# Optimization experiments

Hardware: AMD Instinct MI355X
Metric: run time of the kernel (lower is better)

Reference implementation:

```python
import jax, jax.numpy as jnp
import numpy as np

N_NODES = 100000
N_EDGES = 1600000
D_IN = 128
D_OUT = 128


def setup_inputs() -> dict:
    key = jax.random.key(0)
    k1, k2, k3, k4 = jax.random.split(key, 4)
    feat = jax.random.normal(k1, (N_NODES, D_IN), dtype=jnp.float32)
    W1 = jax.random.normal(k2, (D_OUT, D_IN), dtype=jnp.float32) * (1.0 / np.sqrt(D_IN))
    src = jax.random.randint(k3, (N_EDGES,), 0, N_NODES, dtype=jnp.int32)
    # ensure every dst node has at least one in-edge (no empty segments, like a
    # DGL graph without isolated destination nodes)
    dst_rand = jax.random.randint(k4, (N_EDGES - N_NODES,), 0, N_NODES, dtype=jnp.int32)
    dst = jnp.concatenate([jnp.arange(N_NODES, dtype=jnp.int32), dst_rand])
    return {"feat": feat, "W1": W1, "src": src, "dst": dst}


def reference(feat, W1, src, dst):
    # nn.Linear(bias=False): h = feat @ W1.T   -> [N, D_OUT]
    norm_h = jnp.einsum("nd,od->no", feat, W1)
    # copy_u message + max reduce: segment-max of projected src feats onto dst
    msgs = norm_h[src]                                   # [E, D_OUT] gather
    h_N = jax.ops.segment_max(msgs, dst, num_segments=feat.shape[0])  # [N, D_OUT]
    # concat(feat_dst, h_N) along feature dim
    return jnp.concatenate([feat, h_N], axis=1)          # [N, D_IN + D_OUT]
```

## Files before the change

kernel.cpp:

```cpp
#include <hip/hip_runtime.h>
#include <hip/hip_bf16.h>
#include <cfloat>

typedef short bf16x8 __attribute__((ext_vector_type(8)));
typedef float f32x4 __attribute__((ext_vector_type(4)));

constexpr int NB2     = 1600;
constexpr int PCHUNK  = 6144;
constexpr int NCH_MAX = 264;
constexpr int OFFROW  = 1604;
constexpr int BCAPK   = 2048;

__device__ __forceinline__ unsigned short f32_to_bf16_rne(float f) {
    unsigned int u = __float_as_uint(f);
    u += 0x7fffu + ((u >> 16) & 1u);
    return (unsigned short)(u >> 16);
}
__device__ __forceinline__ float b2f(unsigned int w, int k) {
    return (float)((int)(w << (24 - 8 * k)) >> 24);
}

__global__ __launch_bounds__(256) void ka_part_gemm_kernel(
    const float* __restrict__ feat, const float* __restrict__ W1,
    signed char* __restrict__ norm8, float* __restrict__ rowscale,
    float* __restrict__ out,
    const int* __restrict__ src, const int* __restrict__ dst,
    int* __restrict__ part, unsigned short* __restrict__ offRow,
    int N, int E, int partBlocks) {
    __shared__ __align__(16) char smem[35200];
    const int t = threadIdx.x;

    if ((int)blockIdx.x < partBlocks) {
        int* stage   = (int*)smem;
        int* pkCnt   = stage + PCHUNK;
        int* pkOff   = pkCnt + 800;
        int* pkLoc   = pkOff + 800;
        int* partial = pkLoc + 800;

        const int c0 = blockIdx.x * PCHUNK;
        const int n  = (E - c0 < PCHUNK) ? (E - c0) : PCHUNK;

        for (int i = t; i < 800; i += 256) pkCnt[i] = 0;
        __syncthreads();

#pragma unroll
        for (int j = 0; j < PCHUNK / 1024; ++j) {
            int i = (j * 256 + t) * 4;
            if (i + 3 < n) {
                int4 d4 = *(const int4*)(dst + c0 + i);
                atomicAdd(&pkCnt[(d4.x >> 6) >> 1], 1 << (((d4.x >> 6) & 1) << 4));
                atomicAdd(&pkCnt[(d4.y >> 6) >> 1], 1 << (((d4.y >> 6) & 1) << 4));
                atomicAdd(&pkCnt[(d4.z >> 6) >> 1], 1 << (((d4.z >> 6) & 1) << 4));
                atomicAdd(&pkCnt[(d4.w >> 6) >> 1], 1 << (((d4.w >> 6) & 1) << 4));
            } else if (i < n) {
                for (int k = i; k < n; ++k) {
                    int b = dst[c0 + k] >> 6;
                    atomicAdd(&pkCnt[b >> 1], 1 << ((b & 1) << 4));
                }
            }
        }
        __syncthreads();

        {
            int w0 = 0, w1 = 0, w2 = 0, w3 = 0;
            if (t < 200) {
                w0 = pkCnt[4 * t];     w1 = pkCnt[4 * t + 1];
                w2 = pkCnt[4 * t + 2]; w3 = pkCnt[4 * t + 3];
            }
            int cA = w0 & 0xFFFF, cB = (w0 >> 16) & 0xFFFF;
            int cC = w1 & 0xFFFF, cD = (w1 >> 16) & 0xFFFF;
            int cE = w2 & 0xFFFF, cF = (w2 >> 16) & 0xFFFF;
            int cG = w3 & 0xFFFF, cH = (w3 >> 16) & 0xFFFF;
            partial[t] = cA + cB + cC + cD + cE + cF + cG + cH;
            __syncthreads();
            for (int d = 1; d < 256; d <<= 1) {
                int x = (t >= d) ? partial[t - d] : 0;
                __syncthreads();
                if (t >= d) partial[t] += x;
                __syncthreads();
            }
            if (t < 200) {
                int run = t ? partial[t - 1] : 0;
                int o0 = run,      o1 = o0 + cA, o2 = o1 + cB, o3 = o2 + cC;
                int o4 = o3 + cD,  o5 = o4 + cE, o6 = o5 + cF, o7 = o6 + cG;
                pkOff[4 * t]     = o0 | (o1 << 16);
                pkOff[4 * t + 1] = o2 | (o3 << 16);
                pkOff[4 * t + 2] = o4 | (o5 << 16);
                pkOff[4 * t + 3] = o6 | (o7 << 16);
                pkLoc[4 * t]     = o0 | (o1 << 16);
                pkLoc[4 * t + 1] = o2 | (o3 << 16);
                pkLoc[4 * t + 2] = o4 | (o5 << 16);
                pkLoc[4 * t + 3] = o6 | (o7 << 16);
            }
        }
        __syncthreads();

#pragma unroll
        for (int j = 0; j < PCHUNK / 1024; ++j) {
            int i = (j * 256 + t) * 4;
            if (i + 3 < n) {
                int4 d4 = *(const int4*)(dst + c0 + i);
                int4 s4 = *(const int4*)(src + c0 + i);
                int b, sh, old;
                b = d4.x >> 6; sh = (b & 1) << 4;
                old = atomicAdd(&pkLoc[b >> 1], 1 << sh);
                stage[(old >> sh) & 0xFFFF] = s4.x | ((d4.x & 63) << 17);
                b = d4.y >> 6; sh = (b & 1) << 4;
                old = atomicAdd(&pkLoc[b >> 1], 1 << sh);
                stage[(old >> sh) & 0xFFFF] = s4.y | ((d4.y & 63) << 17);
                b = d4.z >> 6; sh = (b & 1) << 4;
                old = atomicAdd(&pkLoc[b >> 1], 1 << sh);
                stage[(old >> sh) & 0xFFFF] = s4.z | ((d4.z & 63) << 17);
                b = d4.w >> 6; sh = (b & 1) << 4;
                old = atomicAdd(&pkLoc[b >> 1], 1 << sh);
                stage[(old >> sh) & 0xFFFF] = s4.w | ((d4.w & 63) << 17);
            } else if (i < n) {
                for (int k = i; k < n; ++k) {
                    int d = dst[c0 + k];
                    int b = d >> 6, sh = (b & 1) << 4;
                    int old = atomicAdd(&pkLoc[b >> 1], 1 << sh);
                    stage[(old >> sh) & 0xFFFF] = src[c0 + k] | ((d & 63) << 17);
                }
            }
        }
        __syncthreads();

        for (int i = t * 4; i < n; i += 1024) {
            if (i + 3 < n) *(int4*)(part + c0 + i) = *(const int4*)(stage + i);
            else for (int k = i; k < n; ++k) part[c0 + k] = stage[k];
        }
        unsigned short* orow = offRow + (size_t)blockIdx.x * OFFROW;
        for (int b = t; b <= NB2; b += 256) {
            int v = (b < NB2) ? ((pkOff[b >> 1] >> ((b & 1) << 4)) & 0xFFFF) : n;
            orow[b] = (unsigned short)v;
        }
    } else {
        unsigned short* smW = (unsigned short*)smem;
#pragma unroll
        for (int i = 0; i < 8; ++i) {
            int f = i * 256 + t;
            int l = f & 63, kb = (f >> 6) & 3, ot = f >> 8;
            int wrow = ot * 16 + (l & 15);
            int k0 = kb * 32 + (l >> 4) * 8;
            const float* p = W1 + wrow * 128 + k0;
            float4 f0 = *(const float4*)p;
            float4 f1 = *(const float4*)(p + 4);
            union { unsigned short h[8]; uint4 v; } pk;
            pk.h[0] = f32_to_bf16_rne(f0.x); pk.h[1] = f32_to_bf16_rne(f0.y);
            pk.h[2] = f32_to_bf16_rne(f0.z); pk.h[3] = f32_to_bf16_rne(f0.w);
            pk.h[4] = f32_to_bf16_rne(f1.x); pk.h[5] = f32_to_bf16_rne(f1.y);
            pk.h[6] = f32_to_bf16_rne(f1.z); pk.h[7] = f32_to_bf16_rne(f1.w);
            *(uint4*)(smW + (size_t)f * 8) = pk.v;
        }

        const int bid = blockIdx.x - partBlocks;
        const int w = t >> 6;
        const int l = t & 63;
        const int brow0 = bid * 64;
        const int row = brow0 + w * 16 + (l & 15);
        const int kq = (l >> 4) * 8;
        const bool valid = row < N;

        bf16x8 a[4];
        const float* fr = feat + (size_t)row * 128;
        float* orow_ = out + (size_t)row * 256;
#pragma unroll
        for (int kb = 0; kb < 4; ++kb) {
            float4 f0 = make_float4(0.f, 0.f, 0.f, 0.f), f1 = f0;
            if (valid) {
                f0 = *(const float4*)(fr + kb * 32 + kq);
                f1 = *(const float4*)(fr + kb * 32 + kq + 4);
                *(float4*)(orow_ + kb * 32 + kq) = f0;
                *(float4*)(orow_ + kb * 32 + kq + 4) = f1;
            }
            bf16x8 av;
            av[0] = (short)f32_to_bf16_rne(f0.x); av[1] = (short)f32_to_bf16_rne(f0.y);
            av[2] = (short)f32_to_bf16_rne(f0.z); av[3] = (short)f32_to_bf16_rne(f0.w);
            av[4] = (short)f32_to_bf16_rne(f1.x); av[5] = (short)f32_to_bf16_rne(f1.y);
            av[6] = (short)f32_to_bf16_rne(f1.z); av[7] = (short)f32_to_bf16_rne(f1.w);
            a[kb] = av;
        }
        __syncthreads();

        const bf16x8* bfr = (const bf16x8*)smem;
        f32x4 zero = {0.f, 0.f, 0.f, 0.f};
        f32x4 acc[8];
#pragma unroll
        for (int ot = 0; ot < 8; ++ot) acc[ot] = zero;
#pragma unroll
        for (int ot = 0; ot < 8; ++ot) {
#pragma unroll
            for (int kb = 0; kb < 4; ++kb) {
                bf16x8 b = bfr[(ot * 4 + kb) * 64 + l];
                acc[ot] = __builtin_amdgcn_mfma_f32_16x16x32_bf16(a[kb], b, acc[ot], 0, 0, 0);
            }
        }

        const int r0 = w * 16 + (l >> 4) * 4;
        float inv[4], scl[4];
#pragma unroll
        for (int j = 0; j < 4; ++j) {
            float am = 0.f;
#pragma unroll
            for (int ot = 0; ot < 8; ++ot) am = fmaxf(am, __builtin_fabsf(acc[ot][j]));
#pragma unroll
            for (int d = 1; d < 16; d <<= 1) am = fmaxf(am, __shfl_xor(am, d, 64));
            am = fmaxf(am, 1e-30f);
            inv[j] = 127.0f / am;
            scl[j] = am * (1.0f / 127.0f);
        }
        if ((l & 15) == 0) {
#pragma unroll
            for (int j = 0; j < 4; ++j) {
                int grow = brow0 + r0 + j;
                if (grow < N) rowscale[grow] = scl[j];
            }
        }
        __syncthreads();

        char (*sm8)[144] = (char (*)[144])smem;
        const int c0 = l & 15;
#pragma unroll
        for (int ot = 0; ot < 8; ++ot)
#pragma unroll
            for (int j = 0; j < 4; ++j)
                sm8[r0 + j][ot * 16 + c0] = (char)(int)rintf(acc[ot][j] * inv[j]);
        __syncthreads();
#pragma unroll
        for (int i = 0; i < 2; ++i) {
            int idx = i * 256 + t;
            int r = idx >> 3, c = idx & 7;
            int grow = brow0 + r;
            if (grow < N) {
                uint4 v = *(const uint4*)&sm8[r][c * 16];
                *(uint4*)(norm8 + (size_t)grow * 128 + c * 16) = v;
            }
        }
    }
}

__global__ __launch_bounds__(256) void kb_maxpool_kernel(
    const signed char* __restrict__ norm8, const float* __restrict__ rowscale,
    const int* __restrict__ part, const unsigned short* __restrict__ offRow,
    float* __restrict__ out, int N, int nch) {
    __shared__ int eraw[BCAPK];
    __shared__ int esrc[BCAPK];
    __shared__ int runs_s[NCH_MAX];
    __shared__ int rlen[NCH_MAX + 1];
    __shared__ int eoff[65];
    __shared__ int eloc[64];

    const int B = blockIdx.x;
    const int t = threadIdx.x;

    for (int c = t; c < nch; c += 256) {
        const unsigned short* orow = offRow + (size_t)c * OFFROW;
        int s = orow[B];
        int e = orow[B + 1];
        runs_s[c] = s;
        rlen[c] = e - s;
    }
    if (t < 64) eloc[t] = 0;
    __syncthreads();
    if (t < 64) {
        int carry = 0;
        int rounds = (nch + 63) / 64;
        for (int r = 0; r < rounds; ++r) {
            int c = r * 64 + t;
            int orig = (c < nch) ? rlen[c] : 0;
            int v = orig;
#pragma unroll
            for (int d = 1; d < 64; d <<= 1) {
                int x = __shfl_up(v, d, 64);
                if (t >= d) v += x;
            }
            if (c < nch) rlen[c] = carry + v - orig;
            carry += __shfl(v, 63, 64);
        }
        if (t == 0) rlen[nch] = carry;
    }
    __syncthreads();
    int cnt = rlen[nch];
    if (cnt > BCAPK) cnt = BCAPK;

    {
        int g = t >> 4, ln = t & 15;
        for (int c = g; c < nch; c += 16) {
            int s = runs_s[c], d0 = rlen[c], l = rlen[c + 1] - rlen[c];
            const int* gp = part + (size_t)c * PCHUNK + s;
            for (int i = ln; i < l; i += 16) {
                int d = d0 + i;
                if (d < BCAPK) eraw[d] = gp[i];
            }
        }
    }
    __syncthreads();

    for (int i = t; i < cnt; i += 256) atomicAdd(&eloc[eraw[i] >> 17], 1);
    __syncthreads();
    if (t < 64) {
        int v = eloc[t];
        int sc = v;
#pragma unroll
        for (int d = 1; d < 64; d <<= 1) {
            int x = __shfl_up(sc, d, 64);
            if (t >= d) sc += x;
        }
        int excl = sc - v;
        eoff[t] = excl;
        eloc[t] = excl;
        if (t == 63) eoff[64] = sc;
    }
    __syncthreads();
    for (int i = t; i < cnt; i += 256) {
        int v = eraw[i];
        esrc[atomicAdd(&eloc[v >> 17], 1)] = v & 0x1FFFF;
    }
    __syncthreads();

    int qw = t >> 4;
    int ln = t & 15;
    const size_t colb = (size_t)ln * 8;
    for (int dl = qw; dl < 64; dl += 16) {
        int node = (B << 6) + dl;
        if (node >= N) break;
        int si = eoff[dl], se = eoff[dl + 1];
        if (se > BCAPK) se = BCAPK;
        float a0 = -FLT_MAX, a1 = -FLT_MAX, a2 = -FLT_MAX, a3 = -FLT_MAX;
        float a4 = -FLT_MAX, a5 = -FLT_MAX, a6 = -FLT_MAX, a7 = -FLT_MAX;
        float b0 = -FLT_MAX, b1 = -FLT_MAX, b2 = -FLT_MAX, b3 = -FLT_MAX;
        float b4 = -FLT_MAX, b5 = -FLT_MAX, b6 = -FLT_MAX, b7 = -FLT_MAX;
        float c0 = -FLT_MAX, c1 = -FLT_MAX, c2 = -FLT_MAX, c3 = -FLT_MAX;
        float c4 = -FLT_MAX, c5 = -FLT_MAX, c6 = -FLT_MAX, c7 = -FLT_MAX;
        float d0 = -FLT_MAX, d1 = -FLT_MAX, d2 = -FLT_MAX, d3 = -FLT_MAX;
        float d4 = -FLT_MAX, d5 = -FLT_MAX, d6 = -FLT_MAX, d7 = -FLT_MAX;
        int i = si;
        for (; i + 3 < se; i += 4) {
            int s1 = esrc[i], s2 = esrc[i + 1], s3 = esrc[i + 2], s4 = esrc[i + 3];
            uint2 wA = *(const uint2*)(norm8 + (size_t)s1 * 128 + colb);
            uint2 wB = *(const uint2*)(norm8 + (size_t)s2 * 128 + colb);
            uint2 wC = *(const uint2*)(norm8 + (size_t)s3 * 128 + colb);
            uint2 wD = *(const uint2*)(norm8 + (size_t)s4 * 128 + colb);
            float sA = rowscale[s1], sB = rowscale[s2];
            float sC = rowscale[s3], sD = rowscale[s4];
            a0 = fmaxf(a0, b2f(wA.x, 0) * sA); a1 = fmaxf(a1, b2f(wA.x, 1) * sA);
            a2 = fmaxf(a2, b2f(wA.x, 2) * sA); a3 = fmaxf(a3, b2f(wA.x, 3) * sA);
            a4 = fmaxf(a4, b2f(wA.y, 0) * sA); a5 = fmaxf(a5, b2f(wA.y, 1) * sA);
            a6 = fmaxf(a6, b2f(wA.y, 2) * sA); a7 = fmaxf(a7, b2f(wA.y, 3) * sA);
            b0 = fmaxf(b0, b2f(wB.x, 0) * sB); b1 = fmaxf(b1, b2f(wB.x, 1) * sB);
            b2 = fmaxf(b2, b2f(wB.x, 2) * sB); b3 = fmaxf(b3, b2f(wB.x, 3) * sB);
            b4 = fmaxf(b4, b2f(wB.y, 0) * sB); b5 = fmaxf(b5, b2f(wB.y, 1) * sB);
            b6 = fmaxf(b6, b2f(wB.y, 2) * sB); b7 = fmaxf(b7, b2f(wB.y, 3) * sB);
            c0 = fmaxf(c0, b2f(wC.x, 0) * sC); c1 = fmaxf(c1, b2f(wC.x, 1) * sC);
            c2 = fmaxf(c2, b2f(wC.x, 2) * sC); c3 = fmaxf(c3, b2f(wC.x, 3) * sC);
            c4 = fmaxf(c4, b2f(wC.y, 0) * sC); c5 = fmaxf(c5, b2f(wC.y, 1) * sC);
            c6 = fmaxf(c6, b2f(wC.y, 2) * sC); c7 = fmaxf(c7, b2f(wC.y, 3) * sC);
            d0 = fmaxf(d0, b2f(wD.x, 0) * sD); d1 = fmaxf(d1, b2f(wD.x, 1) * sD);
            d2 = fmaxf(d2, b2f(wD.x, 2) * sD); d3 = fmaxf(d3, b2f(wD.x, 3) * sD);
            d4 = fmaxf(d4, b2f(wD.y, 0) * sD); d5 = fmaxf(d5, b2f(wD.y, 1) * sD);
            d6 = fmaxf(d6, b2f(wD.y, 2) * sD); d7 = fmaxf(d7, b2f(wD.y, 3) * sD);
        }
        for (; i < se; ++i) {
            int s1 = esrc[i];
            uint2 wA = *(const uint2*)(norm8 + (size_t)s1 * 128 + colb);
            float sA = rowscale[s1];
            a0 = fmaxf(a0, b2f(wA.x, 0) * sA); a1 = fmaxf(a1, b2f(wA.x, 1) * sA);
            a2 = fmaxf(a2, b2f(wA.x, 2) * sA); a3 = fmaxf(a3, b2f(wA.x, 3) * sA);
            a4 = fmaxf(a4, b2f(wA.y, 0) * sA); a5 = fmaxf(a5, b2f(wA.y, 1) * sA);
            a6 = fmaxf(a6, b2f(wA.y, 2) * sA); a7 = fmaxf(a7, b2f(wA.y, 3) * sA);
        }
        a0 = fmaxf(a0, b0); a1 = fmaxf(a1, b1); a2 = fmaxf(a2, b2); a3 = fmaxf(a3, b3);
        a4 = fmaxf(a4, b4); a5 = fmaxf(a5, b5); a6 = fmaxf(a6, b6); a7 = fmaxf(a7, b7);
        c0 = fmaxf(c0, d0); c1 = fmaxf(c1, d1); c2 = fmaxf(c2, d2); c3 = fmaxf(c3, d3);
        c4 = fmaxf(c4, d4); c5 = fmaxf(c5, d5); c6 = fmaxf(c6, d6); c7 = fmaxf(c7, d7);
        a0 = fmaxf(a0, c0); a1 = fmaxf(a1, c1); a2 = fmaxf(a2, c2); a3 = fmaxf(a3, c3);
        a4 = fmaxf(a4, c4); a5 = fmaxf(a5, c5); a6 = fmaxf(a6, c6); a7 = fmaxf(a7, c7);
        float* op = out + (size_t)node * 256 + 128 + colb;
        *(float4*)op       = make_float4(a0, a1, a2, a3);
        *(float4*)(op + 4) = make_float4(a4, a5, a6, a7);
    }
}

extern "C" void kernel_launch(void* const* d_in, const int* in_sizes, int n_in,
                              void* d_out, int out_size, void* d_ws, size_t ws_size,
                              hipStream_t stream) {
    const float* feat = (const float*)d_in[0];
    const float* W1   = (const float*)d_in[1];
    const int*   src  = (const int*)d_in[2];
    const int*   dst  = (const int*)d_in[3];
    float* out = (float*)d_out;

    const int N = in_sizes[0] / 128;
    const int E = in_sizes[2];
    const int nbk = (N + 63) >> 6;
    const int nchunks = (E + PCHUNK - 1) / PCHUNK;
    const int gemmBlocks = (N + 63) / 64;

    char* wsp = (char*)d_ws;
    size_t o = 0;
    signed char* norm8 = (signed char*)(wsp + o);
    o += ((size_t)N * 128 + 255) & ~(size_t)255;
    float* rowscale = (float*)(wsp + o);
    o += ((size_t)N * 4 + 255) & ~(size_t)255;
    int* part = (int*)(wsp + o);
    o += ((size_t)E * 4 + 255) & ~(size_t)255;
    unsigned short* offRow = (unsigned short*)(wsp + o);
    o += ((size_t)nchunks * OFFROW * 2 + 255) & ~(size_t)255;

    ka_part_gemm_kernel<<<nchunks + gemmBlocks, 256, 0, stream>>>(
        feat, W1, norm8, rowscale, out, src, dst, part, offRow,
        N, E, nchunks);
    kb_maxpool_kernel<<<nbk, 256, 0, stream>>>(
        norm8, rowscale, part, offRow, out, N, nchunks);
}
```

Before: 97.96 us.

## Split maxpool into assemble and pool kernels with register-held edge lists

The per-block gather of partitioned edges moves out of the maxpool kernel into a separate assemble kernel. That kernel writes a contiguous per-block edge list to a new workspace buffer. The maxpool kernel then loads that list into registers (8 per thread), skipping the shared-memory staging array, which cuts LDS use and may raise occupancy. The cost is an extra kernel launch, a global round trip through the new buffer, and an assemble kernel where each thread copies whole runs serially and uncoalesced.

```diff
diff --git a/kernel.cpp b/kernel.cpp
--- a/kernel.cpp
+++ b/kernel.cpp
@@ -10,6 +10,7 @@
 constexpr int NCH_MAX = 264;
 constexpr int OFFROW  = 1604;
 constexpr int BCAPK   = 2048;
+constexpr int EREG2   = 8;
 
 __device__ __forceinline__ unsigned short f32_to_bf16_rne(float f) {
     unsigned int u = __float_as_uint(f);
@@ -239,16 +240,11 @@
     }
 }
 
-__global__ __launch_bounds__(256) void kb_maxpool_kernel(
-    const signed char* __restrict__ norm8, const float* __restrict__ rowscale,
+__global__ __launch_bounds__(256) void km_assemble_kernel(
     const int* __restrict__ part, const unsigned short* __restrict__ offRow,
-    float* __restrict__ out, int N, int nch) {
-    __shared__ int eraw[BCAPK];
-    __shared__ int esrc[BCAPK];
+    int* __restrict__ part2, int* __restrict__ btot2, int nch) {
     __shared__ int runs_s[NCH_MAX];
     __shared__ int rlen[NCH_MAX + 1];
-    __shared__ int eoff[65];
-    __shared__ int eloc[64];
 
     const int B = blockIdx.x;
     const int t = threadIdx.x;
@@ -260,7 +256,6 @@
         runs_s[c] = s;
         rlen[c] = e - s;
     }
-    if (t < 64) eloc[t] = 0;
     __syncthreads();
     if (t < 64) {
         int carry = 0;
@@ -280,23 +275,49 @@
         if (t == 0) rlen[nch] = carry;
     }
     __syncthreads();
-    int cnt = rlen[nch];
+    if (t == 0) btot2[B] = rlen[nch];
+
+    int* dp = part2 + (size_t)B * BCAPK;
+    for (int c = t; c < nch; c += 256) {
+        int s = runs_s[c];
+        int d0 = rlen[c];
+        int len = rlen[c + 1] - d0;
+        const int* gp = part + (size_t)c * PCHUNK + s;
+        for (int i = 0; i < len; ++i) {
+            int d = d0 + i;
+            if (d < BCAPK) dp[d] = gp[i];
+        }
+    }
+}
+
+__global__ __launch_bounds__(256) void kd_maxpool_kernel(
+    const signed char* __restrict__ norm8, const float* __restrict__ rowscale,
+    const int* __restrict__ part2, const int* __restrict__ btot2,
+    float* __restrict__ out, int N) {
+    __shared__ int eoff[65];
+    __shared__ int eloc[64];
+    __shared__ int esrc[BCAPK];
+
+    const int B = blockIdx.x;
+    const int t = threadIdx.x;
+    int cnt = btot2[B];
     if (cnt > BCAPK) cnt = BCAPK;
-
-    {
-        int g = t >> 4, ln = t & 15;
-        for (int c = g; c < nch; c += 16) {
-            int s = runs_s[c], d0 = rlen[c], l = rlen[c + 1] - rlen[c];
-            const int* gp = part + (size_t)c * PCHUNK + s;
-            for (int i = ln; i < l; i += 16) {
-                int d = d0 + i;
-                if (d < BCAPK) eraw[d] = gp[i];
-            }
-        }
-    }
-    __syncthreads();
-
-    for (int i = t; i < cnt; i += 256) atomicAdd(&eloc[eraw[i] >> 17], 1);
+    const int* p = part2 + (size_t)B * BCAPK;
+
+    int ev[EREG2];
+#pragma unroll
+    for (int j = 0; j < EREG2; ++j) {
+        int i = j * 256 + t;
+        ev[j] = (i < cnt) ? p[i] : -1;
+    }
+
+    if (t < 64) eloc[t] = 0;
+    __syncthreads();
+#pragma unroll
+    for (int j = 0; j < EREG2; ++j) {
+        int v = ev[j];
+        if (v >= 0) atomicAdd(&eloc[(v >> 17) & 63], 1);
+    }
     __syncthreads();
     if (t < 64) {
         int v = eloc[t];
@@ -312,9 +333,10 @@
         if (t == 63) eoff[64] = sc;
     }
     __syncthreads();
-    for (int i = t; i < cnt; i += 256) {
-        int v = eraw[i];
-        esrc[atomicAdd(&eloc[v >> 17], 1)] = v & 0x1FFFF;
+#pragma unroll
+    for (int j = 0; j < EREG2; ++j) {
+        int v = ev[j];
+        if (v >= 0) esrc[atomicAdd(&eloc[(v >> 17) & 63], 1)] = v & 0x1FFFF;
     }
     __syncthreads();
 
@@ -325,7 +347,6 @@
         int node = (B << 6) + dl;
         if (node >= N) break;
         int si = eoff[dl], se = eoff[dl + 1];
-        if (se > BCAPK) se = BCAPK;
         float a0 = -FLT_MAX, a1 = -FLT_MAX, a2 = -FLT_MAX, a3 = -FLT_MAX;
         float a4 = -FLT_MAX, a5 = -FLT_MAX, a6 = -FLT_MAX, a7 = -FLT_MAX;
         float b0 = -FLT_MAX, b1 = -FLT_MAX, b2 = -FLT_MAX, b3 = -FLT_MAX;
@@ -406,10 +427,13 @@
     o += ((size_t)E * 4 + 255) & ~(size_t)255;
     unsigned short* offRow = (unsigned short*)(wsp + o);
     o += ((size_t)nchunks * OFFROW * 2 + 255) & ~(size_t)255;
+    int* part2 = (int*)(wsp + o);
+    o += ((size_t)NB2 * BCAPK * 4 + 255) & ~(size_t)255;
+    int* btot2 = (int*)(wsp + o); o += NB2 * 4;
 
     ka_part_gemm_kernel<<<nchunks + gemmBlocks, 256, 0, stream>>>(
         feat, W1, norm8, rowscale, out, src, dst, part, offRow,
         N, E, nchunks);
-    kb_maxpool_kernel<<<nbk, 256, 0, stream>>>(
-        norm8, rowscale, part, offRow, out, N, nchunks);
-}
+    km_assemble_kernel<<<nbk, 256, 0, stream>>>(part, offRow, part2, btot2, nchunks);
+    kd_maxpool_kernel<<<nbk, 256, 0, stream>>>(norm8, rowscale, part2, btot2, out, N);
+}
```

Result: slower. 119.1 us (+21.6%).
